# Kernel tuning notes

Measured on AMD Instinct MI355X. Metric: run time of the kernel, lower is better.

## Reference

```python
import jax, jax.numpy as jnp
import numpy as np

B, S, D = 1, 2048, 4096
N_Q, N_KV, HD = 32, 8, 128
N_REP = N_Q // N_KV
WINDOW = 1024
NEG = -1e9


def setup_inputs() -> dict:
    key = jax.random.key(0)
    ks = jax.random.split(key, 6)
    x = jax.random.normal(ks[0], (B, S, D), dtype=jnp.float32)
    # RoPE frequencies (Llama-style): theta = 10000^{-2i/HD}
    inv_freq = 1.0 / (10000.0 ** (np.arange(0, HD, 2, dtype=np.float32) / HD))
    t = np.arange(S, dtype=np.float32)
    ang = np.outer(t, inv_freq)  # [S, HD//2]
    freqs_cos = jnp.asarray(np.cos(ang), dtype=jnp.float32)
    freqs_sin = jnp.asarray(np.sin(ang), dtype=jnp.float32)
    # additive causal mask [S, S]: 0 on/below diag, -1e9 above
    mask = jnp.where(jnp.tril(jnp.ones((S, S), dtype=bool)), 0.0, NEG).astype(jnp.float32)
    scale = 0.02
    w_q = jax.random.normal(ks[1], (D, N_Q * HD), dtype=jnp.float32) * scale
    w_k = jax.random.normal(ks[2], (D, N_KV * HD), dtype=jnp.float32) * scale
    w_v = jax.random.normal(ks[3], (D, N_KV * HD), dtype=jnp.float32) * scale
    w_o = jax.random.normal(ks[4], (N_Q * HD, D), dtype=jnp.float32) * scale
    return {"x": x, "freqs_cos": freqs_cos, "freqs_sin": freqs_sin, "mask": mask,
            "w_q": w_q, "w_k": w_k, "w_v": w_v, "w_o": w_o}


def _rope(t, cos, sin):
    # t: [B, S, H, HD]; cos/sin: [S, HD//2] -> complex multiply on pairs
    tp = t.reshape(*t.shape[:-1], HD // 2, 2)
    e, o = tp[..., 0], tp[..., 1]
    c = cos[None, :, None, :]
    s = sin[None, :, None, :]
    re = e * c - o * s
    ro = e * s + o * c
    return jnp.stack([re, ro], axis=-1).reshape(t.shape)


def reference(x, freqs_cos, freqs_sin, mask, w_q, w_k, w_v, w_o):
    b, s, _ = x.shape
    xq = (x @ w_q).reshape(b, s, N_Q, HD)
    xk = (x @ w_k).reshape(b, s, N_KV, HD)
    xv = (x @ w_v).reshape(b, s, N_KV, HD)
    xq = _rope(xq, freqs_cos, freqs_sin)
    xk = _rope(xk, freqs_cos, freqs_sin)
    # GQA head repeat
    keys = jnp.repeat(xk, N_REP, axis=2)    # [b, s, N_Q, HD]
    values = jnp.repeat(xv, N_REP, axis=2)
    q = xq.transpose(0, 2, 1, 3)            # [b, h, s, hd]
    k = keys.transpose(0, 2, 1, 3)
    v = values.transpose(0, 2, 1, 3)
    scores = jnp.einsum('bhqd,bhkd->bhqk', q, k) / jnp.sqrt(jnp.float32(HD))
    scores = scores + mask[None, None, :, :]
    # sliding-window band: attend only to keys within WINDOW positions back
    idx = jnp.arange(s)
    diff = idx[:, None] - idx[None, :]
    sliding = (diff >= 0) & (diff < WINDOW)
    scores = jnp.where(sliding[None, None, :, :], scores, NEG)
    probs = jax.nn.softmax(scores, axis=-1).astype(q.dtype)
    out = jnp.einsum('bhqk,bhkd->bhqd', probs, v)
    out = out.transpose(0, 2, 1, 3).reshape(b, s, N_Q * HD)
    return out @ w_o
```

## Files before the change

kernel.cpp:

```cpp
#include <hip/hip_runtime.h>

typedef unsigned short u16;
typedef unsigned int u32;
typedef __bf16 bf16x8 __attribute__((ext_vector_type(8)));
typedef __bf16 bf16x4 __attribute__((ext_vector_type(4)));
typedef float f32x4 __attribute__((ext_vector_type(4)));

#define MFMA16(a, b, c) __builtin_amdgcn_mfma_f32_16x16x32_bf16(a, b, c, 0, 0, 0)

__device__ __forceinline__ u16 f2bf(float f) {
  u32 u = __float_as_uint(f);
  u += 0x7FFFu + ((u >> 16) & 1u);
  return (u16)(u >> 16);
}
__device__ __forceinline__ float bf2f(u16 h) {
  return __uint_as_float(((u32)h) << 16);
}

__device__ __forceinline__ void gload_lds16(const u16* g, u16* l) {
  __builtin_amdgcn_global_load_lds((__attribute__((address_space(1))) void*)g,
                                   (__attribute__((address_space(3))) void*)l,
                                   16, 0, 0);
}

__global__ __launch_bounds__(256) void cvt_x(const float* __restrict__ in,
                                             u16* __restrict__ out) {
  int i = (blockIdx.x * 256 + threadIdx.x) * 4;
  float4 v = *(const float4*)&in[i];
  ushort4 o;
  o.x = f2bf(v.x);
  o.y = f2bf(v.y);
  o.z = f2bf(v.z);
  o.w = f2bf(v.w);
  *(ushort4*)&out[i] = o;
}

__global__ __launch_bounds__(256) void tbf_f2b(const float* __restrict__ in,
                                               u16* __restrict__ out,
                                               int ldin, int ldout) {
  __shared__ float tile[64][65];
  const int t = threadIdx.x;
  const int c4 = t & 15;
  const int rb = t >> 4;
  const int r0 = blockIdx.y * 64;
  const int c0 = blockIdx.x * 64;
#pragma unroll
  for (int p = 0; p < 4; p++) {
    int r = p * 16 + rb;
    float4 v = *(const float4*)&in[(size_t)(r0 + r) * ldin + c0 + c4 * 4];
    tile[r][c4 * 4 + 0] = v.x;
    tile[r][c4 * 4 + 1] = v.y;
    tile[r][c4 * 4 + 2] = v.z;
    tile[r][c4 * 4 + 3] = v.w;
  }
  __syncthreads();
#pragma unroll
  for (int p = 0; p < 4; p++) {
    int oc = p * 16 + rb;
    ushort4 v;
    v.x = f2bf(tile[c4 * 4 + 0][oc]);
    v.y = f2bf(tile[c4 * 4 + 1][oc]);
    v.z = f2bf(tile[c4 * 4 + 2][oc]);
    v.w = f2bf(tile[c4 * 4 + 3][oc]);
    *(ushort4*)&out[(size_t)(c0 + oc) * ldout + r0 + c4 * 4] = v;
  }
}

__global__ __launch_bounds__(256) void tbf_b(const u16* __restrict__ in,
                                             u16* __restrict__ out,
                                             int ldin, int ldout) {
  __shared__ u16 tile[64][68];
  const int t = threadIdx.x;
  const int c4 = t & 15;
  const int rb = t >> 4;
  const int r0 = blockIdx.y * 64;
  const int c0 = blockIdx.x * 64;
#pragma unroll
  for (int p = 0; p < 4; p++) {
    int r = p * 16 + rb;
    ushort4 v = *(const ushort4*)&in[(size_t)(r0 + r) * ldin + c0 + c4 * 4];
    *(ushort4*)&tile[r][c4 * 4] = v;
  }
  __syncthreads();
#pragma unroll
  for (int p = 0; p < 4; p++) {
    int oc = p * 16 + rb;
    ushort4 v;
    v.x = tile[c4 * 4 + 0][oc];
    v.y = tile[c4 * 4 + 1][oc];
    v.z = tile[c4 * 4 + 2][oc];
    v.w = tile[c4 * 4 + 3][oc];
    *(ushort4*)&out[(size_t)(c0 + oc) * ldout + r0 + c4 * 4] = v;
  }
}

template <int BN, int F32OUT>
__global__ __launch_bounds__(512, 2) void gemm8(const u16* __restrict__ A,
                                                const u16* __restrict__ B,
                                                void* __restrict__ Cv,
                                                int K, int ldc) {
  constexpr int NC = BN / 64;
  __shared__ __attribute__((aligned(16))) u16 As[2][256 * 64];
  __shared__ __attribute__((aligned(16))) u16 Bs[2][BN * 64];
  const int tid = threadIdx.x;
  const int wave = tid >> 6;
  const int lane = tid & 63;
  const int l16 = lane & 15;
  const int quad = lane >> 4;
  const int wm = wave >> 2;
  const int wc = wave & 3;
  const int id = blockIdx.x;
  const int bm = (id & 7) * 256;
  const int bn0 = (id >> 3) * BN;

  const u16* srcA[4];
#pragma unroll
  for (int m = 0; m < 4; m++) {
    int c = m * 512 + tid;
    int r = c >> 3;
    int hl = (c & 7) ^ (r & 7);
    srcA[m] = A + (size_t)(bm + r) * K + hl * 8;
  }
  const u16* srcB[NC];
#pragma unroll
  for (int m = 0; m < NC; m++) {
    int c = m * 512 + tid;
    int r = c >> 3;
    int hl = (c & 7) ^ (r & 7);
    srcB[m] = B + (size_t)(bn0 + r) * K + hl * 8;
  }

  f32x4 acc[8][NC];
#pragma unroll
  for (int i = 0; i < 8; i++)
#pragma unroll
    for (int j = 0; j < NC; j++) acc[i][j] = (f32x4){0.f, 0.f, 0.f, 0.f};

#define STA(u, koff, buf) \
  gload_lds16(srcA[u] + (koff), &As[buf][((u) * 512 + tid) * 8])
#define STB(u, koff, buf) \
  gload_lds16(srcB[u] + (koff), &Bs[buf][((u) * 512 + tid) * 8])
#define SB __builtin_amdgcn_sched_barrier(0)
#define MID                                          \
  SB;                                                \
  __builtin_amdgcn_s_barrier();                      \
  asm volatile("s_waitcnt lgkmcnt(0)" ::: "memory"); \
  SB
#define END                     \
  SB;                           \
  __builtin_amdgcn_s_barrier(); \
  SB

  bf16x8 aR[2][4], bR0[NC], bR1[NC];
  auto rdA = [&](const u16* s, int mh) {
#pragma unroll
    for (int ks = 0; ks < 2; ks++)
#pragma unroll
      for (int ii = 0; ii < 4; ii++) {
        int row = wm * 128 + mh * 64 + ii * 16 + l16;
        aR[ks][ii] = *(const bf16x8*)
            &s[row * 64 + (((ks * 4 + quad) ^ (row & 7)) << 3)];
      }
  };
  auto rdB = [&](const u16* s, int ks, bf16x8(&bR)[NC]) {
#pragma unroll
    for (int j = 0; j < NC; j++) {
      int row = wc * (NC * 16) + j * 16 + l16;
      bR[j] = *(const bf16x8*)
          &s[row * 64 + (((ks * 4 + quad) ^ (row & 7)) << 3)];
    }
  };
  auto cl = [&](bf16x8(&a4)[4], bf16x8(&bR)[NC], int mh) {
    __builtin_amdgcn_s_setprio(1);
#pragma unroll
    for (int ii = 0; ii < 4; ii++)
#pragma unroll
      for (int j = 0; j < NC; j++)
        acc[mh * 4 + ii][j] = MFMA16(a4[ii], bR[j], acc[mh * 4 + ii][j]);
    __builtin_amdgcn_s_setprio(0);
  };

#pragma unroll
  for (int u = 0; u < 4; u++) STA(u, 0, 0);
#pragma unroll
  for (int u = 0; u < NC; u++) STB(u, 0, 0);
#pragma unroll
  for (int u = 0; u < NC; u++) STB(u, 64, 1);
  if constexpr (NC == 3)
    asm volatile("s_waitcnt vmcnt(3)" ::: "memory");
  else
    asm volatile("s_waitcnt vmcnt(2)" ::: "memory");
  END;

  const int NP = K >> 7;
  for (int p = 0; p < NP; ++p) {
    const int kT1 = p * 128 + 64;
    const int kT2 = p * 128 + 128;
    const int kT3 = p * 128 + 192;
    const bool more = (p + 1 < NP);
    const u16* as0 = &As[0][0];
    const u16* bs0 = &Bs[0][0];
    const u16* as1 = &As[1][0];
    const u16* bs1 = &Bs[1][0];

    rdA(as0, 0);
    rdB(bs0, 0, bR0);
    STA(0, kT1, 1);
    STA(1, kT1, 1);
    MID;
    cl(aR[0], bR0, 0);
    END;
    rdB(bs0, 1, bR1);
    STA(2, kT1, 1);
    STA(3, kT1, 1);
    MID;
    cl(aR[1], bR1, 0);
    END;
    rdA(as0, 1);
    if (more) {
      STB(0, kT2, 0);
      STB(1, kT2, 0);
    }
    MID;
    cl(aR[1], bR1, 1);
    END;
    if (more) {
      if constexpr (NC == 3) {
        STB(2, kT2, 0);
        STA(0, kT2, 0);
      } else {
        STA(0, kT2, 0);
        STA(1, kT2, 0);
      }
    }
    MID;
    cl(aR[0], bR0, 1);
    SB;
    if (more)
      asm volatile("s_waitcnt vmcnt(4)" ::: "memory");
    else
      asm volatile("s_waitcnt vmcnt(0)" ::: "memory");
    END;

    rdA(as1, 0);
    rdB(bs1, 0, bR0);
    if (more) {
      if constexpr (NC == 3) {
        STA(1, kT2, 0);
        STA(2, kT2, 0);
      } else {
        STA(2, kT2, 0);
        STA(3, kT2, 0);
      }
    }
    MID;
    cl(aR[0], bR0, 0);
    END;
    rdB(bs1, 1, bR1);
    if (more) {
      if constexpr (NC == 3) STA(3, kT2, 0);
    }
    MID;
    cl(aR[1], bR1, 0);
    END;
    rdA(as1, 1);
    if (more) {
      STB(0, kT3, 1);
      STB(1, kT3, 1);
    }
    MID;
    cl(aR[1], bR1, 1);
    END;
    if (more) {
      if constexpr (NC == 3) STB(2, kT3, 1);
    }
    MID;
    cl(aR[0], bR0, 1);
    SB;
    if (more) {
      if constexpr (NC == 3)
        asm volatile("s_waitcnt vmcnt(3)" ::: "memory");
      else
        asm volatile("s_waitcnt vmcnt(2)" ::: "memory");
    }
    END;
  }

  const int crow0 = bm + wm * 128;
  const int ccol0 = bn0 + wc * (NC * 16);
  if constexpr (F32OUT) {
    float* Cp = (float*)Cv;
#pragma unroll
    for (int r8 = 0; r8 < 8; r8++)
#pragma unroll
      for (int j = 0; j < NC; j++)
#pragma unroll
        for (int rr = 0; rr < 4; rr++) {
          int row = crow0 + (r8 >> 2) * 64 + (r8 & 3) * 16 + quad * 4 + rr;
          int col = ccol0 + j * 16 + l16;
          Cp[(size_t)row * ldc + col] = acc[r8][j][rr];
        }
  } else {
    u16* Cp = (u16*)Cv;
#pragma unroll
    for (int r8 = 0; r8 < 8; r8++)
#pragma unroll
      for (int j = 0; j < NC; j++)
#pragma unroll
        for (int rr = 0; rr < 4; rr++) {
          int row = crow0 + (r8 >> 2) * 64 + (r8 & 3) * 16 + quad * 4 + rr;
          int col = ccol0 + j * 16 + l16;
          Cp[(size_t)row * ldc + col] = f2bf(acc[r8][j][rr]);
        }
  }
#undef STA
#undef STB
#undef SB
#undef MID
#undef END
}

__global__ __launch_bounds__(256) void rope_k(u16* __restrict__ qkv,
                                              const float* __restrict__ fc,
                                              const float* __restrict__ fs) {
  int idx = blockIdx.x * 256 + threadIdx.x;
  int j = idx & 63;
  int rem = idx >> 6;
  int head = rem % 40;
  int s = rem / 40;
  float c = fc[s * 64 + j];
  float sn = fs[s * 64 + j];
  int col = (head < 32) ? (head * 128 + 2 * j) : (4096 + (head - 32) * 128 + 2 * j);
  u32* p = (u32*)&qkv[(size_t)s * 6144 + col];
  u32 v = *p;
  float e = bf2f((u16)(v & 0xFFFFu));
  float o = bf2f((u16)(v >> 16));
  float re = e * c - o * sn;
  float ro = e * sn + o * c;
  *p = (u32)f2bf(re) | ((u32)f2bf(ro) << 16);
}

__global__ __launch_bounds__(256) void attn_k(const u16* __restrict__ qkv,
                                              const u16* __restrict__ vt,
                                              u16* __restrict__ outb) {
  __shared__ __attribute__((aligned(16))) u16 Kb[2][32 * 128];
  __shared__ __attribute__((aligned(16))) u16 Vb[2][128 * 32];
  __shared__ __attribute__((aligned(16))) u16 plds[4][32 * 36];
  const int h = blockIdx.x;
  const int q0 = blockIdx.y * 128;
  const int t = threadIdx.x;
  const int wave = t >> 6;
  const int lane = t & 63;
  const int l16 = lane & 15;
  const int quad = lane >> 4;
  const int hkv = h >> 2;
  const int qw = q0 + wave * 32;
  u16* myp = &plds[wave][0];

  bf16x8 qa[2][4];
#pragma unroll
  for (int i = 0; i < 2; i++)
#pragma unroll
    for (int kc = 0; kc < 4; kc++)
      qa[i][kc] = *(const bf16x8*)&qkv[(size_t)(qw + i * 16 + l16) * 6144 +
                                       h * 128 + kc * 32 + quad * 8];

  f32x4 o[2][8];
#pragma unroll
  for (int i = 0; i < 2; i++)
#pragma unroll
    for (int d = 0; d < 8; d++) o[i][d] = (f32x4){0.f, 0.f, 0.f, 0.f};
  float lloc[2][4] = {{0.f, 0.f, 0.f, 0.f}, {0.f, 0.f, 0.f, 0.f}};

  const int kb_start = (q0 - 1023 > 0 ? q0 - 1023 : 0) & ~31;
  const int kb_last = q0 + 96;
  const float sc = 0.08838834764831845f;

  const int kr0 = t >> 4, kc0s = t & 15;
  const int kr1 = (256 + t) >> 4, kc1s = t & 15;
  const int vr0 = t >> 2, vc0s = t & 3;
  const int vr1 = (256 + t) >> 2, vc1s = t & 3;
  const u16* kg = qkv + 4096 + hkv * 128;
  const u16* vg = vt + (size_t)hkv * 128 * 2048;

#define STAGE(kb_, nb_)                                                        \
  do {                                                                         \
    int kb__ = (kb_);                                                          \
    gload_lds16(&kg[(size_t)(kb__ + kr0) * 6144 + (kc0s ^ (kr0 & 15)) * 8],    \
                &Kb[nb_][t * 8]);                                              \
    gload_lds16(&kg[(size_t)(kb__ + kr1) * 6144 + (kc1s ^ (kr1 & 15)) * 8],    \
                &Kb[nb_][2048 + t * 8]);                                       \
    gload_lds16(&vg[(size_t)vr0 * 2048 + kb__ + (vc0s ^ (vr0 & 3)) * 8],       \
                &Vb[nb_][t * 8]);                                              \
    gload_lds16(&vg[(size_t)vr1 * 2048 + kb__ + (vc1s ^ (vr1 & 3)) * 8],       \
                &Vb[nb_][2048 + t * 8]);                                       \
  } while (0)

  STAGE(kb_start, 0);
  int cur = 0;

  for (int kb = kb_start; kb <= kb_last; kb += 32) {
    __syncthreads();
    if (kb + 32 <= kb_last) STAGE(kb + 32, cur ^ 1);
    const u16* kcur = &Kb[cur][0];
    const u16* vcur = &Vb[cur][0];

    f32x4 s0[2] = {(f32x4){0.f, 0.f, 0.f, 0.f}, (f32x4){0.f, 0.f, 0.f, 0.f}};
    f32x4 s1[2] = {(f32x4){0.f, 0.f, 0.f, 0.f}, (f32x4){0.f, 0.f, 0.f, 0.f}};
#pragma unroll
    for (int kc = 0; kc < 4; kc++) {
      int ch = ((kc * 4 + quad) ^ l16) * 8;
      bf16x8 b0 = *(const bf16x8*)&kcur[l16 * 128 + ch];
      bf16x8 b1 = *(const bf16x8*)&kcur[(l16 + 16) * 128 + ch];
      s0[0] = MFMA16(qa[0][kc], b0, s0[0]);
      s1[0] = MFMA16(qa[0][kc], b1, s1[0]);
      s0[1] = MFMA16(qa[1][kc], b0, s0[1]);
      s1[1] = MFMA16(qa[1][kc], b1, s1[1]);
    }

    float p0[2][4], p1[2][4];
    bool fast = (kb + 31 <= qw) && (qw + 31 - kb <= 1023);
    if (fast) {
#pragma unroll
      for (int i = 0; i < 2; i++)
#pragma unroll
        for (int r = 0; r < 4; r++) {
          p0[i][r] = __expf(s0[i][r] * sc);
          p1[i][r] = __expf(s1[i][r] * sc);
        }
    } else {
#pragma unroll
      for (int i = 0; i < 2; i++)
#pragma unroll
        for (int r = 0; r < 4; r++) {
          int row = qw + i * 16 + quad * 4 + r;
          int col0 = kb + l16;
          int col1 = col0 + 16;
          bool v0 = (col0 <= row) && (row - col0 < 1024);
          bool v1 = (col1 <= row) && (row - col1 < 1024);
          p0[i][r] = v0 ? __expf(s0[i][r] * sc) : 0.f;
          p1[i][r] = v1 ? __expf(s1[i][r] * sc) : 0.f;
        }
    }
#pragma unroll
    for (int i = 0; i < 2; i++)
#pragma unroll
      for (int r = 0; r < 4; r++) {
        lloc[i][r] += p0[i][r] + p1[i][r];
        myp[(i * 16 + quad * 4 + r) * 36 + l16] = f2bf(p0[i][r]);
        myp[(i * 16 + quad * 4 + r) * 36 + l16 + 16] = f2bf(p1[i][r]);
      }
    asm volatile("s_waitcnt lgkmcnt(0)" ::: "memory");
    bf16x8 pa[2];
#pragma unroll
    for (int i = 0; i < 2; i++) {
      bf16x4 lo = *(const bf16x4*)&myp[(i * 16 + l16) * 36 + quad * 8];
      bf16x4 hi = *(const bf16x4*)&myp[(i * 16 + l16) * 36 + quad * 8 + 4];
#pragma unroll
      for (int j = 0; j < 4; j++) {
        pa[i][j] = lo[j];
        pa[i][j + 4] = hi[j];
      }
    }
#pragma unroll
    for (int d = 0; d < 8; d++) {
      int rv = l16 + 16 * d;
      bf16x8 vb = *(const bf16x8*)&vcur[rv * 32 + ((quad ^ (l16 & 3)) * 8)];
      o[0][d] = MFMA16(pa[0], vb, o[0][d]);
      o[1][d] = MFMA16(pa[1], vb, o[1][d]);
    }
    cur ^= 1;
  }

#pragma unroll
  for (int i = 0; i < 2; i++) {
    float inv[4];
#pragma unroll
    for (int r = 0; r < 4; r++) {
      float l = lloc[i][r];
#pragma unroll
      for (int m = 8; m >= 1; m >>= 1) l += __shfl_xor(l, m, 64);
      inv[r] = 1.0f / l;
    }
#pragma unroll
    for (int d = 0; d < 8; d++)
#pragma unroll
      for (int r = 0; r < 4; r++) {
        int row = qw + i * 16 + quad * 4 + r;
        outb[(size_t)row * 4096 + h * 128 + d * 16 + l16] =
            f2bf(o[i][d][r] * inv[r]);
      }
  }
#undef STAGE
}

extern "C" void kernel_launch(void* const* d_in, const int* in_sizes, int n_in,
                              void* d_out, int out_size, void* d_ws, size_t ws_size,
                              hipStream_t stream) {
  const float* x = (const float*)d_in[0];
  const float* fc = (const float*)d_in[1];
  const float* fs = (const float*)d_in[2];
  const float* wq = (const float*)d_in[4];
  const float* wk = (const float*)d_in[5];
  const float* wv = (const float*)d_in[6];
  const float* wo = (const float*)d_in[7];
  float* outp = (float*)d_out;
  char* ws = (char*)d_ws;
  u16* xb = (u16*)(ws);
  u16* wqkvT = (u16*)(ws + 16777216);
  u16* qkvb = (u16*)(ws + 67108864);
  u16* vtb = (u16*)(ws + 92274688);
  u16* aout = (u16*)(ws + 96468992);

  cvt_x<<<8192, 256, 0, stream>>>(x, xb);
  tbf_f2b<<<dim3(64, 64), 256, 0, stream>>>(wq, wqkvT, 4096, 4096);
  tbf_f2b<<<dim3(16, 64), 256, 0, stream>>>(wk, wqkvT + (size_t)4096 * 4096,
                                            1024, 4096);
  tbf_f2b<<<dim3(16, 64), 256, 0, stream>>>(wv, wqkvT + (size_t)5120 * 4096,
                                            1024, 4096);
  gemm8<192, 0><<<256, 512, 0, stream>>>(xb, wqkvT, qkvb, 4096, 6144);
  rope_k<<<20480, 256, 0, stream>>>(qkvb, fc, fs);
  tbf_b<<<dim3(16, 32), 256, 0, stream>>>(qkvb + 5120, vtb, 6144, 2048);
  tbf_f2b<<<dim3(64, 64), 256, 0, stream>>>(wo, wqkvT, 4096, 4096);
  attn_k<<<dim3(32, 16), 256, 0, stream>>>(qkvb, vtb, aout);
  gemm8<128, 1><<<256, 512, 0, stream>>>(aout, wqkvT, outp, 4096, 4096);
}
```

Before: 481.0 us.

## Enlarge attention tiles to 256 queries and 64-key blocks with per-wave skipping

The attention kernel now runs 512 threads (8 waves) per block covering 256 queries, and stages 64-key K/V tiles with a wider XOR swizzle. Each K/V tile loaded into LDS is shared by twice as many query rows, and each barrier covers twice as many keys. Waves whose rows fall entirely outside a tile's causal or window range now skip its compute. MFMA priority hints and a scheduling barrier are added. In exchange the grid shrinks to 256 blocks, so GPU occupancy drops, and waves wait on each other at the shared barrier.

```diff
diff --git a/kernel.cpp b/kernel.cpp
--- a/kernel.cpp
+++ b/kernel.cpp
@@ -340,14 +340,14 @@
   *p = (u32)f2bf(re) | ((u32)f2bf(ro) << 16);
 }
 
-__global__ __launch_bounds__(256) void attn_k(const u16* __restrict__ qkv,
+__global__ __launch_bounds__(512) void attn_k(const u16* __restrict__ qkv,
                                               const u16* __restrict__ vt,
                                               u16* __restrict__ outb) {
-  __shared__ __attribute__((aligned(16))) u16 Kb[2][32 * 128];
-  __shared__ __attribute__((aligned(16))) u16 Vb[2][128 * 32];
-  __shared__ __attribute__((aligned(16))) u16 plds[4][32 * 36];
+  __shared__ __attribute__((aligned(16))) u16 Kb[2][64 * 128];
+  __shared__ __attribute__((aligned(16))) u16 Vb[2][128 * 64];
+  __shared__ __attribute__((aligned(16))) u16 plds[8][32 * 72];
   const int h = blockIdx.x;
-  const int q0 = blockIdx.y * 128;
+  const int q0 = blockIdx.y * 256;
   const int t = threadIdx.x;
   const int wave = t >> 6;
   const int lane = t & 63;
@@ -372,102 +372,115 @@
     for (int d = 0; d < 8; d++) o[i][d] = (f32x4){0.f, 0.f, 0.f, 0.f};
   float lloc[2][4] = {{0.f, 0.f, 0.f, 0.f}, {0.f, 0.f, 0.f, 0.f}};
 
-  const int kb_start = (q0 - 1023 > 0 ? q0 - 1023 : 0) & ~31;
-  const int kb_last = q0 + 96;
+  const int kb_start = (q0 - 1023 > 0 ? q0 - 1023 : 0) & ~63;
+  const int kb_last = q0 + 192;
   const float sc = 0.08838834764831845f;
 
-  const int kr0 = t >> 4, kc0s = t & 15;
-  const int kr1 = (256 + t) >> 4, kc1s = t & 15;
-  const int vr0 = t >> 2, vc0s = t & 3;
-  const int vr1 = (256 + t) >> 2, vc1s = t & 3;
+  const int kr0 = t >> 4, ks0 = t & 15;
+  const int kr1 = (512 + t) >> 4, ks1 = t & 15;
+  const int vr0 = t >> 3, vs0 = t & 7;
+  const int vr1 = (512 + t) >> 3, vs1 = t & 7;
   const u16* kg = qkv + 4096 + hkv * 128;
   const u16* vg = vt + (size_t)hkv * 128 * 2048;
 
-#define STAGE(kb_, nb_)                                                        \
-  do {                                                                         \
-    int kb__ = (kb_);                                                          \
-    gload_lds16(&kg[(size_t)(kb__ + kr0) * 6144 + (kc0s ^ (kr0 & 15)) * 8],    \
-                &Kb[nb_][t * 8]);                                              \
-    gload_lds16(&kg[(size_t)(kb__ + kr1) * 6144 + (kc1s ^ (kr1 & 15)) * 8],    \
-                &Kb[nb_][2048 + t * 8]);                                       \
-    gload_lds16(&vg[(size_t)vr0 * 2048 + kb__ + (vc0s ^ (vr0 & 3)) * 8],       \
-                &Vb[nb_][t * 8]);                                              \
-    gload_lds16(&vg[(size_t)vr1 * 2048 + kb__ + (vc1s ^ (vr1 & 3)) * 8],       \
-                &Vb[nb_][2048 + t * 8]);                                       \
+#define STAGE(kb_, nb_)                                                       \
+  do {                                                                        \
+    int kb__ = (kb_);                                                         \
+    gload_lds16(&kg[(size_t)(kb__ + kr0) * 6144 + (ks0 ^ (kr0 & 15)) * 8],    \
+                &Kb[nb_][t * 8]);                                             \
+    gload_lds16(&kg[(size_t)(kb__ + kr1) * 6144 + (ks1 ^ (kr1 & 15)) * 8],    \
+                &Kb[nb_][4096 + t * 8]);                                      \
+    gload_lds16(&vg[(size_t)vr0 * 2048 + kb__ + (vs0 ^ (vr0 & 7)) * 8],       \
+                &Vb[nb_][t * 8]);                                             \
+    gload_lds16(&vg[(size_t)vr1 * 2048 + kb__ + (vs1 ^ (vr1 & 7)) * 8],       \
+                &Vb[nb_][4096 + t * 8]);                                      \
   } while (0)
 
   STAGE(kb_start, 0);
   int cur = 0;
 
-  for (int kb = kb_start; kb <= kb_last; kb += 32) {
+  for (int kb = kb_start; kb <= kb_last; kb += 64) {
     __syncthreads();
-    if (kb + 32 <= kb_last) STAGE(kb + 32, cur ^ 1);
+    if (kb + 64 <= kb_last) STAGE(kb + 64, cur ^ 1);
+    if (kb > qw + 31 || kb + 1087 <= qw) {
+      cur ^= 1;
+      continue;
+    }
     const u16* kcur = &Kb[cur][0];
     const u16* vcur = &Vb[cur][0];
 
-    f32x4 s0[2] = {(f32x4){0.f, 0.f, 0.f, 0.f}, (f32x4){0.f, 0.f, 0.f, 0.f}};
-    f32x4 s1[2] = {(f32x4){0.f, 0.f, 0.f, 0.f}, (f32x4){0.f, 0.f, 0.f, 0.f}};
+    f32x4 s[2][4];
+#pragma unroll
+    for (int i = 0; i < 2; i++)
+#pragma unroll
+      for (int kt = 0; kt < 4; kt++) s[i][kt] = (f32x4){0.f, 0.f, 0.f, 0.f};
 #pragma unroll
     for (int kc = 0; kc < 4; kc++) {
       int ch = ((kc * 4 + quad) ^ l16) * 8;
-      bf16x8 b0 = *(const bf16x8*)&kcur[l16 * 128 + ch];
-      bf16x8 b1 = *(const bf16x8*)&kcur[(l16 + 16) * 128 + ch];
-      s0[0] = MFMA16(qa[0][kc], b0, s0[0]);
-      s1[0] = MFMA16(qa[0][kc], b1, s1[0]);
-      s0[1] = MFMA16(qa[1][kc], b0, s0[1]);
-      s1[1] = MFMA16(qa[1][kc], b1, s1[1]);
-    }
-
-    float p0[2][4], p1[2][4];
-    bool fast = (kb + 31 <= qw) && (qw + 31 - kb <= 1023);
+      bf16x8 bfr[4];
+#pragma unroll
+      for (int kt = 0; kt < 4; kt++)
+        bfr[kt] = *(const bf16x8*)&kcur[(kt * 16 + l16) * 128 + ch];
+      __builtin_amdgcn_s_setprio(1);
+#pragma unroll
+      for (int kt = 0; kt < 4; kt++) {
+        s[0][kt] = MFMA16(qa[0][kc], bfr[kt], s[0][kt]);
+        s[1][kt] = MFMA16(qa[1][kc], bfr[kt], s[1][kt]);
+      }
+      __builtin_amdgcn_s_setprio(0);
+    }
+
+    float p[2][4][4];
+    bool fast = (kb + 63 <= qw) && (qw + 31 - kb <= 1023);
     if (fast) {
 #pragma unroll
       for (int i = 0; i < 2; i++)
 #pragma unroll
-        for (int r = 0; r < 4; r++) {
-          p0[i][r] = __expf(s0[i][r] * sc);
-          p1[i][r] = __expf(s1[i][r] * sc);
-        }
+        for (int kt = 0; kt < 4; kt++)
+#pragma unroll
+          for (int r = 0; r < 4; r++) p[i][kt][r] = __expf(s[i][kt][r] * sc);
     } else {
 #pragma unroll
       for (int i = 0; i < 2; i++)
 #pragma unroll
-        for (int r = 0; r < 4; r++) {
-          int row = qw + i * 16 + quad * 4 + r;
-          int col0 = kb + l16;
-          int col1 = col0 + 16;
-          bool v0 = (col0 <= row) && (row - col0 < 1024);
-          bool v1 = (col1 <= row) && (row - col1 < 1024);
-          p0[i][r] = v0 ? __expf(s0[i][r] * sc) : 0.f;
-          p1[i][r] = v1 ? __expf(s1[i][r] * sc) : 0.f;
-        }
+        for (int kt = 0; kt < 4; kt++)
+#pragma unroll
+          for (int r = 0; r < 4; r++) {
+            int row = qw + i * 16 + quad * 4 + r;
+            int col = kb + kt * 16 + l16;
+            bool v = (col <= row) && (row - col < 1024);
+            p[i][kt][r] = v ? __expf(s[i][kt][r] * sc) : 0.f;
+          }
     }
 #pragma unroll
     for (int i = 0; i < 2; i++)
 #pragma unroll
       for (int r = 0; r < 4; r++) {
-        lloc[i][r] += p0[i][r] + p1[i][r];
-        myp[(i * 16 + quad * 4 + r) * 36 + l16] = f2bf(p0[i][r]);
-        myp[(i * 16 + quad * 4 + r) * 36 + l16 + 16] = f2bf(p1[i][r]);
+        lloc[i][r] += (p[i][0][r] + p[i][1][r]) + (p[i][2][r] + p[i][3][r]);
+#pragma unroll
+        for (int kt = 0; kt < 4; kt++)
+          myp[(i * 16 + quad * 4 + r) * 72 + kt * 16 + l16] =
+              f2bf(p[i][kt][r]);
       }
     asm volatile("s_waitcnt lgkmcnt(0)" ::: "memory");
-    bf16x8 pa[2];
-#pragma unroll
-    for (int i = 0; i < 2; i++) {
-      bf16x4 lo = *(const bf16x4*)&myp[(i * 16 + l16) * 36 + quad * 8];
-      bf16x4 hi = *(const bf16x4*)&myp[(i * 16 + l16) * 36 + quad * 8 + 4];
-#pragma unroll
-      for (int j = 0; j < 4; j++) {
-        pa[i][j] = lo[j];
-        pa[i][j + 4] = hi[j];
-      }
-    }
-#pragma unroll
-    for (int d = 0; d < 8; d++) {
-      int rv = l16 + 16 * d;
-      bf16x8 vb = *(const bf16x8*)&vcur[rv * 32 + ((quad ^ (l16 & 3)) * 8)];
-      o[0][d] = MFMA16(pa[0], vb, o[0][d]);
-      o[1][d] = MFMA16(pa[1], vb, o[1][d]);
+    __builtin_amdgcn_sched_barrier(0);
+    bf16x8 pa[2][2];
+#pragma unroll
+    for (int i = 0; i < 2; i++)
+#pragma unroll
+      for (int kh = 0; kh < 2; kh++)
+        pa[i][kh] = *(const bf16x8*)&myp[(i * 16 + l16) * 72 + kh * 32 +
+                                         quad * 8];
+#pragma unroll
+    for (int kh = 0; kh < 2; kh++) {
+#pragma unroll
+      for (int d = 0; d < 8; d++) {
+        int rv = l16 + 16 * d;
+        bf16x8 vb = *(const bf16x8*)
+            &vcur[rv * 64 + (((kh * 4 + quad) ^ (rv & 7)) * 8)];
+        o[0][d] = MFMA16(pa[0][kh], vb, o[0][d]);
+        o[1][d] = MFMA16(pa[1][kh], vb, o[1][d]);
+      }
     }
     cur ^= 1;
   }
@@ -522,6 +535,6 @@
   rope_k<<<20480, 256, 0, stream>>>(qkvb, fc, fs);
   tbf_b<<<dim3(16, 32), 256, 0, stream>>>(qkvb + 5120, vtb, 6144, 2048);
   tbf_f2b<<<dim3(64, 64), 256, 0, stream>>>(wo, wqkvT, 4096, 4096);
-  attn_k<<<dim3(32, 16), 256, 0, stream>>>(qkvb, vtb, aout);
+  attn_k<<<dim3(32, 8), 512, 0, stream>>>(qkvb, vtb, aout);
   gemm8<128, 1><<<256, 512, 0, stream>>>(aout, wqkvT, outp, 4096, 4096);
 }
```

New measurement: 478.4 us. No clear change (-0.5%).
